# Performance work log

Measured on AMD Instinct MI355X. Metric: run time of the kernel, lower is better.

## Reference

```python
import jax, jax.numpy as jnp
import numpy as np

D_MODEL = 1024
NUM_HEADS = 16
HEAD_DIM = D_MODEL // NUM_HEADS


def setup_inputs() -> dict:
    key = jax.random.key(0)
    ks = jax.random.split(key, 6)
    B, S = 2, 2048
    s = 1.0 / np.sqrt(D_MODEL)
    return {
        "x": jax.random.normal(ks[0], (B, S, D_MODEL), dtype=jnp.float32),
        "Wq": jax.random.normal(ks[1], (D_MODEL, D_MODEL), dtype=jnp.float32) * s,
        "Wk": jax.random.normal(ks[2], (D_MODEL, D_MODEL), dtype=jnp.float32) * s,
        "Wv": jax.random.normal(ks[3], (D_MODEL, D_MODEL), dtype=jnp.float32) * s,
        "Wo": jax.random.normal(ks[4], (D_MODEL, D_MODEL), dtype=jnp.float32) * s,
        "bo": jax.random.normal(ks[5], (D_MODEL,), dtype=jnp.float32) * 0.01,
    }


def reference(x, Wq, Wk, Wv, Wo, bo):
    b, n, _ = x.shape
    # QKV projections (no bias, qkv_bias=False); weights applied as x @ W^T like nn.Linear
    q = (x @ Wq.T).reshape(b, n, NUM_HEADS, HEAD_DIM).transpose(0, 2, 1, 3)  # [b,h,n,d]
    k = (x @ Wk.T).reshape(b, n, NUM_HEADS, HEAD_DIM).transpose(0, 2, 1, 3)
    v = (x @ Wv.T).reshape(b, n, NUM_HEADS, HEAD_DIM).transpose(0, 2, 1, 3)
    scores = jnp.einsum("bhqd,bhkd->bhqk", q, k)
    causal = jnp.tril(jnp.ones((n, n), dtype=bool))  # keep where True
    scores = jnp.where(causal, scores, -jnp.inf)
    weights = jax.nn.softmax(scores / np.sqrt(HEAD_DIM), axis=-1)
    # dropout p=0.0 -> identity (eval semantics)
    ctx = jnp.einsum("bhqk,bhkd->bhqd", weights, v)
    ctx = ctx.transpose(0, 2, 1, 3).reshape(b, n, D_MODEL)
    return ctx @ Wo.T + bo
```

## Files before the change

### kernel.cpp

```cpp
#include <hip/hip_runtime.h>

#define D_MODEL 1024
#define NUM_HEADS 16
#define HEAD_DIM 64
#define BATCH 2
#define SEQ 2048
#define MTOT (BATCH * SEQ)

typedef __attribute__((ext_vector_type(8))) short bf16x8;
typedef __attribute__((ext_vector_type(4))) short s16x4;
typedef __attribute__((ext_vector_type(4))) float f32x4;
typedef unsigned short u16;
typedef unsigned long long u64;

__device__ __forceinline__ u16 f2bf(float f) {
    unsigned u = __float_as_uint(f);
    return (u16)((u + 0x7FFFu + ((u >> 16) & 1u)) >> 16);
}
__device__ __forceinline__ float bf2f(u16 v) {
    return __uint_as_float((unsigned)v << 16);
}

__device__ __forceinline__ unsigned cvt_pk_bf16(float lo, float hi) {
    unsigned r;
    asm volatile("v_cvt_pk_bf16_f32 %0, %1, %2" : "=v"(r) : "v"(lo), "v"(hi));
    return r;
}

#if __has_builtin(__builtin_amdgcn_exp2f)
#define EXP2(x) __builtin_amdgcn_exp2f(x)
#else
#define EXP2(x) exp2f(x)
#endif

#define GLOAD16(gp, lp) __builtin_amdgcn_global_load_lds(                      \
    (const __attribute__((address_space(1))) void*)(gp),                       \
    (__attribute__((address_space(3))) void*)(lp), 16, 0, 0)

__global__ __launch_bounds__(256)
void cast_all_kernel(const float* __restrict__ x,  const float* __restrict__ Wq,
                     const float* __restrict__ Wk, const float* __restrict__ Wv,
                     const float* __restrict__ Wo, u16* __restrict__ dst)
{
    const int i = blockIdx.x * 256 + threadIdx.x;
    const float* src;
    int j;
    if (i < 524288) { src = x; j = i; }
    else if (i < 917504) {
        const int k = i - 524288;
        const int z = k >> 17;
        src = (z == 0) ? Wq : (z == 1) ? Wk : Wv;
        j = k & 0x1FFFF;
    } else { src = Wo; j = i - 917504; }
    const float4* s = reinterpret_cast<const float4*>(src) + (size_t)j * 2;
    float4 a = s[0], b = s[1];
    u16 tmp[8] = {f2bf(a.x), f2bf(a.y), f2bf(a.z), f2bf(a.w),
                  f2bf(b.x), f2bf(b.y), f2bf(b.z), f2bf(b.w)};
    *reinterpret_cast<int4*>(dst + (size_t)i * 8) = *reinterpret_cast<int4*>(tmp);
}

__global__ __launch_bounds__(512, 4)
void gemm_qkv_kernel(const u16* __restrict__ A, const u16* __restrict__ B,
                     u16* __restrict__ Qo, u16* __restrict__ Ko, u16* __restrict__ Vt)
{
    __shared__ u16 Al[3][128 * 32];
    __shared__ u16 Bl[3][256 * 32];

    const int tid = threadIdx.x;
    const int l = tid & 63;
    const int w = tid >> 6;
    const int wm = w >> 2, wn = w & 3;
    const int lr = l & 15, lg = l >> 4;

    const int bid = blockIdx.x;
    const int swz = (bid & 7) * 48 + (bid >> 3);
    const int mb = swz / 12, nb = swz % 12;
    const int m0 = mb * 128, n0 = nb * 256;

    const int arow = tid >> 2;
    const int acol = ((tid & 3) ^ ((arow >> 1) & 3)) * 8;
    const int br1  = (512 + tid) >> 2;
    const int bcol1 = ((tid & 3) ^ ((br1 >> 1) & 3)) * 8;
    const int dst0 = tid * 8;
    const int dst1 = 4096 + tid * 8;
    const int rsw = (lr >> 1) & 3;

    f32x4 acc[4][4];
    #pragma unroll
    for (int i = 0; i < 4; ++i)
        #pragma unroll
        for (int j = 0; j < 4; ++j) acc[i][j] = (f32x4){0.f, 0.f, 0.f, 0.f};

    #pragma unroll
    for (int t = 0; t < 2; ++t) {
        const int k0 = t * 32;
        GLOAD16(A + (size_t)(m0 + arow) * D_MODEL + k0 + acol,  &Al[t][dst0]);
        GLOAD16(B + (size_t)(n0 + arow) * D_MODEL + k0 + acol,  &Bl[t][dst0]);
        GLOAD16(B + (size_t)(n0 + br1)  * D_MODEL + k0 + bcol1, &Bl[t][dst1]);
    }

    int cb = 0;
    for (int t = 0; t < 32; ++t) {
        if (t < 31) asm volatile("s_waitcnt vmcnt(3)" ::: "memory");
        else        asm volatile("s_waitcnt vmcnt(0)" ::: "memory");
        __builtin_amdgcn_s_barrier();

        if (t + 2 < 32) {
            const int sb = (cb >= 1) ? cb - 1 : cb + 2;
            const int k0 = (t + 2) * 32;
            GLOAD16(A + (size_t)(m0 + arow) * D_MODEL + k0 + acol,  &Al[sb][dst0]);
            GLOAD16(B + (size_t)(n0 + arow) * D_MODEL + k0 + acol,  &Bl[sb][dst0]);
            GLOAD16(B + (size_t)(n0 + br1)  * D_MODEL + k0 + bcol1, &Bl[sb][dst1]);
        }

        const u16* __restrict__ Ab = Al[cb];
        const u16* __restrict__ Bb = Bl[cb];
        bf16x8 af[4], bfr[4];
        #pragma unroll
        for (int i = 0; i < 4; ++i)
            af[i] = *reinterpret_cast<const bf16x8*>(
                &Ab[(wm * 64 + i * 16 + lr) * 32 + ((lg ^ rsw) * 8)]);
        #pragma unroll
        for (int j = 0; j < 4; ++j)
            bfr[j] = *reinterpret_cast<const bf16x8*>(
                &Bb[(wn * 64 + j * 16 + lr) * 32 + ((lg ^ rsw) * 8)]);

        __builtin_amdgcn_s_setprio(1);
        #pragma unroll
        for (int i = 0; i < 4; ++i)
            #pragma unroll
            for (int j = 0; j < 4; ++j)
                acc[i][j] = __builtin_amdgcn_mfma_f32_16x16x32_bf16(
                    af[i], bfr[j], acc[i][j], 0, 0, 0);
        __builtin_amdgcn_s_setprio(0);

        cb = (cb == 2) ? 0 : cb + 1;
    }

    const int z = (n0 >> 10);
    if (z < 2) {
        #pragma unroll
        for (int i = 0; i < 4; ++i) {
            #pragma unroll
            for (int r = 0; r < 4; ++r) {
                const int m = m0 + wm * 64 + i * 16 + lg * 4 + r;
                const int bb = m >> 11, s = m & (SEQ - 1);
                #pragma unroll
                for (int j = 0; j < 4; ++j) {
                    const int c = n0 + wn * 64 + j * 16 + lr;
                    const int cc = c & 1023, h = cc >> 6, d = cc & 63;
                    const size_t idx = ((size_t)(bb * NUM_HEADS + h) * SEQ + s) * 64 + d;
                    if (z == 0) Qo[idx] = f2bf(acc[i][j][r] * 0.18033688f);
                    else        Ko[idx] = f2bf(acc[i][j][r]);
                }
            }
        }
    } else {
        #pragma unroll
        for (int i = 0; i < 4; ++i) {
            const int mbase = m0 + wm * 64 + i * 16 + lg * 4;
            const int bb = mbase >> 11, s = mbase & (SEQ - 1);
            #pragma unroll
            for (int j = 0; j < 4; ++j) {
                const int c = n0 + wn * 64 + j * 16 + lr;
                const int cc = c & 1023, h = cc >> 6, d = cc & 63;
                u16 t4[4];
                #pragma unroll
                for (int r = 0; r < 4; ++r) t4[r] = f2bf(acc[i][j][r]);
                *reinterpret_cast<u64*>(
                    &Vt[((size_t)(bb * NUM_HEADS + h) * 64 + d) * SEQ + s]) =
                    *reinterpret_cast<u64*>(t4);
            }
        }
    }
}

__global__ __launch_bounds__(256)
void gemm_out_kernel(const u16* __restrict__ A, const u16* __restrict__ B,
                     const float* __restrict__ bias, float* __restrict__ out)
{
    __shared__ u16 Al[128 * 64];
    __shared__ u16 Bl[128 * 64];

    const int tid = threadIdx.x;
    const int l = tid & 63;
    const int w = tid >> 6;
    const int wm = w >> 1, wn = w & 1;
    const int lr = l & 15, lg = l >> 4;
    const int m0 = blockIdx.y * 128;
    const int n0 = blockIdx.x * 128;

    const int srow = tid >> 3;
    const int scol = ((tid & 7) ^ (srow & 7)) * 8;
    const int sxa = (lr & 7) * 8;

    f32x4 acc[4][4];
    #pragma unroll
    for (int i = 0; i < 4; ++i)
        #pragma unroll
        for (int j = 0; j < 4; ++j) acc[i][j] = (f32x4){0.f, 0.f, 0.f, 0.f};

    for (int k0 = 0; k0 < D_MODEL; k0 += 64) {
        __syncthreads();
        #pragma unroll
        for (int i = 0; i < 4; ++i) {
            const u16* ga = A + (size_t)(m0 + i * 32 + srow) * D_MODEL + k0 + scol;
            const u16* gb = B + (size_t)(n0 + i * 32 + srow) * D_MODEL + k0 + scol;
            GLOAD16(ga, Al + i * 2048 + w * 512);
            GLOAD16(gb, Bl + i * 2048 + w * 512);
        }
        __syncthreads();
        #pragma unroll
        for (int kc = 0; kc < 2; ++kc) {
            bf16x8 af[4], bfr[4];
            #pragma unroll
            for (int i = 0; i < 4; ++i)
                af[i] = *reinterpret_cast<const bf16x8*>(
                    &Al[(wm * 64 + i * 16 + lr) * 64 + ((kc * 32 + lg * 8) ^ sxa)]);
            #pragma unroll
            for (int j = 0; j < 4; ++j)
                bfr[j] = *reinterpret_cast<const bf16x8*>(
                    &Bl[(wn * 64 + j * 16 + lr) * 64 + ((kc * 32 + lg * 8) ^ sxa)]);
            #pragma unroll
            for (int i = 0; i < 4; ++i)
                #pragma unroll
                for (int j = 0; j < 4; ++j)
                    acc[i][j] = __builtin_amdgcn_mfma_f32_16x16x32_bf16(
                        af[i], bfr[j], acc[i][j], 0, 0, 0);
        }
    }

    #pragma unroll
    for (int i = 0; i < 4; ++i) {
        #pragma unroll
        for (int r = 0; r < 4; ++r) {
            const int m = m0 + wm * 64 + i * 16 + lg * 4 + r;
            #pragma unroll
            for (int j = 0; j < 4; ++j) {
                const int c = n0 + wn * 64 + j * 16 + lr;
                out[(size_t)m * D_MODEL + c] = acc[i][j][r] + bias[c];
            }
        }
    }
}

__device__ __forceinline__ void map_pair128(int p, int& qt2, int& ch) {
    if (p < 16)      { qt2 = 15 - (p >> 2); ch = p & 3; }
    else if (p < 28) { int t = p - 16; qt2 = 11 - t / 3; ch = t % 3; }
    else if (p < 36) { int t = p - 28; qt2 = 7 - (t >> 1); ch = t & 1; }
    else             { qt2 = 39 - p; ch = 0; }
}

__global__ __launch_bounds__(256)
void attn_kernel(const u16* __restrict__ Q, const u16* __restrict__ K,
                 const u16* __restrict__ Vt, u16* __restrict__ ctx,
                 u16* __restrict__ Opart, float* __restrict__ Lpart)
{
    __shared__ char LdsB[2][16384];

    const int tid = threadIdx.x;
    const int l = tid & 63;
    const int w = tid >> 6;
    const int lr = l & 15;
    const int lg = l >> 4;

    const int xcd  = blockIdx.x & 7;
    const int slot = blockIdx.x >> 3;
    const int bh   = xcd * 4 + slot / 40;
    int qt2, ch;
    map_pair128(slot % 40, qt2, ch);

    const int ntiles = 2 * qt2 + 2;
    const int nch  = (ntiles + 7) >> 3;
    const int base = ntiles / nch, rem = ntiles % nch;
    const int start = ch * base + (ch < rem ? ch : rem);
    const int cnt   = base + (ch < rem ? 1 : 0);

    const size_t hbase = (size_t)bh * SEQ * 64;
    const int b = bh >> 4, h = bh & (NUM_HEADS - 1);
    const u16* __restrict__ Kh = K + hbase;
    const u16* __restrict__ Vh = Vt + hbase;
    const int q0 = qt2 * 128;

    const int r0 = tid >> 3;
    const int c0 = ((tid & 7) ^ (r0 & 7)) * 8;
    const int r1 = (256 + tid) >> 3;
    const int c1 = ((tid & 7) ^ (r1 & 7)) * 8;
    const int d0b = tid * 16;
    const int d1b = 4096 + tid * 16;
    const int rswz = (lr & 7) << 4;

    bf16x8 qf[2][2];
    #pragma unroll
    for (int fq = 0; fq < 2; ++fq) {
        const u16* qp = Q + hbase + (size_t)(q0 + fq * 64 + w * 16 + lr) * 64 + lg * 8;
        qf[fq][0] = *reinterpret_cast<const bf16x8*>(qp);
        qf[fq][1] = *reinterpret_cast<const bf16x8*>(qp + 32);
    }
    asm volatile("s_waitcnt vmcnt(0)" ::: "memory");

    f32x4 acc[2][4];
    #pragma unroll
    for (int fq = 0; fq < 2; ++fq)
        #pragma unroll
        for (int nb = 0; nb < 4; ++nb) acc[fq][nb] = (f32x4){0.f, 0.f, 0.f, 0.f};
    float lsumv[2] = {0.f, 0.f};

    {
        char* kb = LdsB[0];
        char* vb = LdsB[0] + 8192;
        const int kb64 = start * 64;
        GLOAD16(Kh + (size_t)(kb64 + r0) * 64 + c0, kb + d0b);
        GLOAD16(Kh + (size_t)(kb64 + r1) * 64 + c1, kb + d1b);
        GLOAD16(Vh + (size_t)r0 * SEQ + kb64 + c0, vb + d0b);
        GLOAD16(Vh + (size_t)r1 * SEQ + kb64 + c1, vb + d1b);
    }

    for (int it = 0; it < cnt; ++it) {
        const int tile = start + it;
        const int buf = it & 1;
        if (it < cnt - 1) {
            const int kb64 = (tile + 1) * 64;
            char* kbl = LdsB[buf ^ 1];
            char* vbl = kbl + 8192;
            GLOAD16(Kh + (size_t)(kb64 + r0) * 64 + c0, kbl + d0b);
            GLOAD16(Kh + (size_t)(kb64 + r1) * 64 + c1, kbl + d1b);
            GLOAD16(Vh + (size_t)r0 * SEQ + kb64 + c0, vbl + d0b);
            GLOAD16(Vh + (size_t)r1 * SEQ + kb64 + c1, vbl + d1b);
            asm volatile("s_waitcnt vmcnt(4)" ::: "memory");
        } else {
            asm volatile("s_waitcnt vmcnt(0)" ::: "memory");
        }
        __builtin_amdgcn_s_barrier();

        const char* kbuf = LdsB[buf];
        const char* vbuf = kbuf + 8192;

        bf16x8 kf[4][2];
        #pragma unroll
        for (int m = 0; m < 4; ++m) {
            const char* krow = kbuf + (16 * m + lr) * 128;
            kf[m][0] = *reinterpret_cast<const bf16x8*>(krow + ((lg * 16) ^ rswz));
            kf[m][1] = *reinterpret_cast<const bf16x8*>(krow + ((64 + lg * 16) ^ rswz));
        }

        const bool diag = (tile >= 2 * qt2);
        const int koff0 = (tile - 2 * qt2) * 64;

        unsigned dw[2][4][2];
        __builtin_amdgcn_s_setprio(1);
        #pragma unroll
        for (int fq = 0; fq < 2; ++fq) {
            f32x4 s[4];
            #pragma unroll
            for (int m = 0; m < 4; ++m) {
                s[m] = (f32x4){0.f, 0.f, 0.f, 0.f};
                s[m] = __builtin_amdgcn_mfma_f32_16x16x32_bf16(kf[m][0], qf[fq][0], s[m], 0, 0, 0);
                s[m] = __builtin_amdgcn_mfma_f32_16x16x32_bf16(kf[m][1], qf[fq][1], s[m], 0, 0, 0);
            }
            if (diag) {
                const int qloc = fq * 64 + w * 16 + lr;
                #pragma unroll
                for (int m = 0; m < 4; ++m)
                    #pragma unroll
                    for (int r = 0; r < 4; ++r)
                        if (koff0 + 16 * m + 4 * lg + r > qloc) s[m][r] = -1.0e38f;
            }
            float p[4][4];
            #pragma unroll
            for (int m = 0; m < 4; ++m) {
                #pragma unroll
                for (int r = 0; r < 4; ++r) p[m][r] = EXP2(s[m][r]);
                lsumv[fq] += (p[m][0] + p[m][1]) + (p[m][2] + p[m][3]);
                dw[fq][m][0] = cvt_pk_bf16(p[m][0], p[m][1]);
                dw[fq][m][1] = cvt_pk_bf16(p[m][2], p[m][3]);
            }
        }

        #pragma unroll
        for (int c = 0; c < 2; ++c) {
            union Pu { unsigned u[4]; bf16x8 v; } pb[2];
            #pragma unroll
            for (int fq = 0; fq < 2; ++fq) {
                pb[fq].u[0] = dw[fq][2 * c][0];     pb[fq].u[1] = dw[fq][2 * c][1];
                pb[fq].u[2] = dw[fq][2 * c + 1][0]; pb[fq].u[3] = dw[fq][2 * c + 1][1];
            }
            #pragma unroll
            for (int nb = 0; nb < 4; ++nb) {
                const char* vrow = vbuf + (16 * nb + lr) * 128;
                union Vu { s16x4 hv[2]; bf16x8 v; } vf;
                vf.hv[0] = *reinterpret_cast<const s16x4*>(
                    vrow + ((c * 64 + lg * 8) ^ rswz));
                vf.hv[1] = *reinterpret_cast<const s16x4*>(
                    vrow + ((c * 64 + 32 + lg * 8) ^ rswz));
                acc[0][nb] = __builtin_amdgcn_mfma_f32_16x16x32_bf16(
                    vf.v, pb[0].v, acc[0][nb], 0, 0, 0);
                acc[1][nb] = __builtin_amdgcn_mfma_f32_16x16x32_bf16(
                    vf.v, pb[1].v, acc[1][nb], 0, 0, 0);
            }
        }
        __builtin_amdgcn_s_setprio(0);

        __builtin_amdgcn_s_barrier();
    }

    #pragma unroll
    for (int fq = 0; fq < 2; ++fq) {
        lsumv[fq] += __shfl_xor(lsumv[fq], 16);
        lsumv[fq] += __shfl_xor(lsumv[fq], 32);
    }

    if (nch == 1) {
        #pragma unroll
        for (int fq = 0; fq < 2; ++fq) {
            const float inv = 1.0f / lsumv[fq];
            const int qrow = q0 + fq * 64 + w * 16 + lr;
            u16* op = ctx + ((size_t)(b * SEQ) + qrow) * D_MODEL + h * 64 + 4 * lg;
            #pragma unroll
            for (int nb = 0; nb < 4; ++nb) {
                u16 t4[4];
                #pragma unroll
                for (int r = 0; r < 4; ++r) t4[r] = f2bf(acc[fq][nb][r] * inv);
                *reinterpret_cast<u64*>(op + 16 * nb) = *reinterpret_cast<u64*>(t4);
            }
        }
    } else {
        const int slot4 = ((bh * 12 + (qt2 - 4)) << 2) + ch;
        #pragma unroll
        for (int fq = 0; fq < 2; ++fq) {
            const int rloc = fq * 64 + w * 16 + lr;
            u16* op = Opart + (size_t)slot4 * 8192 + rloc * 64 + 4 * lg;
            #pragma unroll
            for (int nb = 0; nb < 4; ++nb) {
                u16 t4[4];
                #pragma unroll
                for (int r = 0; r < 4; ++r) t4[r] = f2bf(acc[fq][nb][r]);
                *reinterpret_cast<u64*>(op + 16 * nb) = *reinterpret_cast<u64*>(t4);
            }
            if (lg == 0) Lpart[slot4 * 128 + rloc] = lsumv[fq];
        }
    }
}

__global__ __launch_bounds__(128)
void attn_reduce_kernel(const u16* __restrict__ Opart,
                        const float* __restrict__ Lpart,
                        u16* __restrict__ ctx)
{
    const int blk = blockIdx.x;
    const int bh = blk / 12, idx = blk % 12;
    const int qt2 = idx + 4;
    const int nch = (2 * qt2 + 2 + 7) >> 3;
    const int t = threadIdx.x;
    const int b = bh >> 4, h = bh & (NUM_HEADS - 1);
    const int slot0 = (bh * 12 + idx) << 2;

    float acc[64] = {};
    float lt = 0.f;
    for (int ch = 0; ch < nch; ++ch) {
        const u16* op = Opart + (size_t)(slot0 + ch) * 8192 + t * 64;
        lt += Lpart[(slot0 + ch) * 128 + t];
        #pragma unroll
        for (int cchunk = 0; cchunk < 8; ++cchunk) {
            u16 v[8];
            *reinterpret_cast<int4*>(v) =
                *reinterpret_cast<const int4*>(op + cchunk * 8);
            #pragma unroll
            for (int j = 0; j < 8; ++j) acc[cchunk * 8 + j] += bf2f(v[j]);
        }
    }
    const float inv = 1.0f / lt;
    u16* orow = ctx + ((size_t)(b * SEQ) + qt2 * 128 + t) * D_MODEL + h * 64;
    #pragma unroll
    for (int cchunk = 0; cchunk < 8; ++cchunk) {
        u16 v[8];
        #pragma unroll
        for (int j = 0; j < 8; ++j) v[j] = f2bf(acc[cchunk * 8 + j] * inv);
        *reinterpret_cast<int4*>(orow + cchunk * 8) = *reinterpret_cast<int4*>(v);
    }
}


extern "C" void kernel_launch(void* const* d_in, const int* in_sizes, int n_in,
                              void* d_out, int out_size, void* d_ws, size_t ws_size,
                              hipStream_t stream)
{
    const float* x  = (const float*)d_in[0];
    const float* Wq = (const float*)d_in[1];
    const float* Wk = (const float*)d_in[2];
    const float* Wv = (const float*)d_in[3];
    const float* Wo = (const float*)d_in[4];
    const float* bo = (const float*)d_in[5];
    float* out = (float*)d_out;

    u16* xb   = (u16*)d_ws;
    u16* wqkv = xb   + (size_t)MTOT * D_MODEL;
    u16* wob  = wqkv + (size_t)3 * D_MODEL * D_MODEL;
    u16* Qw   = wob  + (size_t)D_MODEL * D_MODEL;
    u16* Kw   = Qw   + (size_t)MTOT * D_MODEL;
    u16* Vtw  = Kw   + (size_t)MTOT * D_MODEL;
    u16* ctxb = Vtw  + (size_t)MTOT * D_MODEL;
    u16* Opart = ctxb + (size_t)MTOT * D_MODEL;
    float* Lpart = (float*)(Opart + (size_t)1536 * 8192);

    cast_all_kernel<<<4096, 256, 0, stream>>>(x, Wq, Wk, Wv, Wo, xb);

    gemm_qkv_kernel<<<dim3(384), 512, 0, stream>>>(xb, wqkv, Qw, Kw, Vtw);

    attn_kernel<<<dim3(1280), 256, 0, stream>>>(Qw, Kw, Vtw, ctxb, Opart, Lpart);
    attn_reduce_kernel<<<dim3(384), 128, 0, stream>>>(Opart, Lpart, ctxb);

    dim3 go(D_MODEL / 128, MTOT / 128);
    gemm_out_kernel<<<go, 256, 0, stream>>>(ctxb, wob, bo, out);
}
```

Before: 118.6 us.

## Triple-buffer out-projection GEMM, swizzle block order, restructure attention barriers

```diff
diff --git a/kernel.cpp b/kernel.cpp
--- a/kernel.cpp
+++ b/kernel.cpp
@@ -175,24 +175,31 @@
     }
 }
 
-__global__ __launch_bounds__(256)
+__global__ __launch_bounds__(256, 3)
 void gemm_out_kernel(const u16* __restrict__ A, const u16* __restrict__ B,
                      const float* __restrict__ bias, float* __restrict__ out)
 {
-    __shared__ u16 Al[128 * 64];
-    __shared__ u16 Bl[128 * 64];
+    __shared__ u16 Al[3][128 * 32];
+    __shared__ u16 Bl[3][128 * 32];
 
     const int tid = threadIdx.x;
     const int l = tid & 63;
     const int w = tid >> 6;
     const int wm = w >> 1, wn = w & 1;
     const int lr = l & 15, lg = l >> 4;
-    const int m0 = blockIdx.y * 128;
-    const int n0 = blockIdx.x * 128;
-
-    const int srow = tid >> 3;
-    const int scol = ((tid & 7) ^ (srow & 7)) * 8;
-    const int sxa = (lr & 7) * 8;
+
+    const int bid = blockIdx.x;
+    const int swz = (bid & 7) * 32 + (bid >> 3);
+    const int mb = swz >> 3, nb = swz & 7;
+    const int m0 = mb * 128, n0 = nb * 128;
+
+    const int r0 = tid >> 2;
+    const int c0 = ((tid & 3) ^ ((r0 >> 1) & 3)) * 8;
+    const int r1 = 64 + (tid >> 2);
+    const int c1 = ((tid & 3) ^ ((r1 >> 1) & 3)) * 8;
+    const int dst0 = tid * 8;
+    const int dst1 = 2048 + tid * 8;
+    const int rsw = (lr >> 1) & 3;
 
     f32x4 acc[4][4];
     #pragma unroll
@@ -200,34 +207,52 @@
         #pragma unroll
         for (int j = 0; j < 4; ++j) acc[i][j] = (f32x4){0.f, 0.f, 0.f, 0.f};
 
-    for (int k0 = 0; k0 < D_MODEL; k0 += 64) {
-        __syncthreads();
-        #pragma unroll
-        for (int i = 0; i < 4; ++i) {
-            const u16* ga = A + (size_t)(m0 + i * 32 + srow) * D_MODEL + k0 + scol;
-            const u16* gb = B + (size_t)(n0 + i * 32 + srow) * D_MODEL + k0 + scol;
-            GLOAD16(ga, Al + i * 2048 + w * 512);
-            GLOAD16(gb, Bl + i * 2048 + w * 512);
-        }
-        __syncthreads();
-        #pragma unroll
-        for (int kc = 0; kc < 2; ++kc) {
-            bf16x8 af[4], bfr[4];
-            #pragma unroll
-            for (int i = 0; i < 4; ++i)
-                af[i] = *reinterpret_cast<const bf16x8*>(
-                    &Al[(wm * 64 + i * 16 + lr) * 64 + ((kc * 32 + lg * 8) ^ sxa)]);
+    #pragma unroll
+    for (int t = 0; t < 2; ++t) {
+        const int k0 = t * 32;
+        GLOAD16(A + (size_t)(m0 + r0) * D_MODEL + k0 + c0, &Al[t][dst0]);
+        GLOAD16(A + (size_t)(m0 + r1) * D_MODEL + k0 + c1, &Al[t][dst1]);
+        GLOAD16(B + (size_t)(n0 + r0) * D_MODEL + k0 + c0, &Bl[t][dst0]);
+        GLOAD16(B + (size_t)(n0 + r1) * D_MODEL + k0 + c1, &Bl[t][dst1]);
+    }
+
+    int cb = 0;
+    for (int t = 0; t < 32; ++t) {
+        if (t < 31) asm volatile("s_waitcnt vmcnt(4)" ::: "memory");
+        else        asm volatile("s_waitcnt vmcnt(0)" ::: "memory");
+        __builtin_amdgcn_s_barrier();
+
+        if (t + 2 < 32) {
+            const int sb = (cb >= 1) ? cb - 1 : cb + 2;
+            const int k0 = (t + 2) * 32;
+            GLOAD16(A + (size_t)(m0 + r0) * D_MODEL + k0 + c0, &Al[sb][dst0]);
+            GLOAD16(A + (size_t)(m0 + r1) * D_MODEL + k0 + c1, &Al[sb][dst1]);
+            GLOAD16(B + (size_t)(n0 + r0) * D_MODEL + k0 + c0, &Bl[sb][dst0]);
+            GLOAD16(B + (size_t)(n0 + r1) * D_MODEL + k0 + c1, &Bl[sb][dst1]);
+        }
+
+        const u16* __restrict__ Ab = Al[cb];
+        const u16* __restrict__ Bb = Bl[cb];
+        bf16x8 af[4], bfr[4];
+        #pragma unroll
+        for (int i = 0; i < 4; ++i)
+            af[i] = *reinterpret_cast<const bf16x8*>(
+                &Ab[(wm * 64 + i * 16 + lr) * 32 + ((lg ^ rsw) * 8)]);
+        #pragma unroll
+        for (int j = 0; j < 4; ++j)
+            bfr[j] = *reinterpret_cast<const bf16x8*>(
+                &Bb[(wn * 64 + j * 16 + lr) * 32 + ((lg ^ rsw) * 8)]);
+
+        __builtin_amdgcn_s_setprio(1);
+        #pragma unroll
+        for (int i = 0; i < 4; ++i)
             #pragma unroll
             for (int j = 0; j < 4; ++j)
-                bfr[j] = *reinterpret_cast<const bf16x8*>(
-                    &Bl[(wn * 64 + j * 16 + lr) * 64 + ((kc * 32 + lg * 8) ^ sxa)]);
-            #pragma unroll
-            for (int i = 0; i < 4; ++i)
-                #pragma unroll
-                for (int j = 0; j < 4; ++j)
-                    acc[i][j] = __builtin_amdgcn_mfma_f32_16x16x32_bf16(
-                        af[i], bfr[j], acc[i][j], 0, 0, 0);
-        }
+                acc[i][j] = __builtin_amdgcn_mfma_f32_16x16x32_bf16(
+                    af[i], bfr[j], acc[i][j], 0, 0, 0);
+        __builtin_amdgcn_s_setprio(0);
+
+        cb = (cb == 2) ? 0 : cb + 1;
     }
 
     #pragma unroll
@@ -319,6 +344,10 @@
     for (int it = 0; it < cnt; ++it) {
         const int tile = start + it;
         const int buf = it & 1;
+
+        asm volatile("s_waitcnt vmcnt(0)" ::: "memory");
+        __builtin_amdgcn_s_barrier();
+
         if (it < cnt - 1) {
             const int kb64 = (tile + 1) * 64;
             char* kbl = LdsB[buf ^ 1];
@@ -327,11 +356,7 @@
             GLOAD16(Kh + (size_t)(kb64 + r1) * 64 + c1, kbl + d1b);
             GLOAD16(Vh + (size_t)r0 * SEQ + kb64 + c0, vbl + d0b);
             GLOAD16(Vh + (size_t)r1 * SEQ + kb64 + c1, vbl + d1b);
-            asm volatile("s_waitcnt vmcnt(4)" ::: "memory");
-        } else {
-            asm volatile("s_waitcnt vmcnt(0)" ::: "memory");
-        }
-        __builtin_amdgcn_s_barrier();
+        }
 
         const char* kbuf = LdsB[buf];
         const char* vbuf = kbuf + 8192;
@@ -400,8 +425,6 @@
             }
         }
         __builtin_amdgcn_s_setprio(0);
-
-        __builtin_amdgcn_s_barrier();
     }
 
     #pragma unroll
@@ -511,5 +534,5 @@
     attn_reduce_kernel<<<dim3(384), 128, 0, stream>>>(Opart, Lpart, ctxb);
 
     dim3 go(D_MODEL / 128, MTOT / 128);
-    gemm_out_kernel<<<go, 256, 0, stream>>>(ctxb, wob, bo, out);
-}
+    gemm_out_kernel<<<go.x * go.y, 256, 0, stream>>>(ctxb, wob, bo, out);
+}
```

Measured after the change: 117.1 us. About the same (-1.3%).
